# Optimization experiments

Measured on AMD Instinct MI355X. Metric: run time of the kernel, lower is better.

Reference implementation:

```python
import jax, jax.numpy as jnp
import numpy as np

B, T, E, A = 4, 4096, 1024, 1024

def setup_inputs() -> dict:
    key = jax.random.key(0)
    k1, k2, k3, k4 = jax.random.split(key, 4)
    scale = 1.0 / np.sqrt(E)  # ~ nn.Linear default init scale
    return {
        "embedded": jax.random.normal(k1, (B, T, E), dtype=jnp.float32),
        "Wq": jax.random.uniform(k2, (A, E), jnp.float32, -scale, scale),
        "Wk": jax.random.uniform(k3, (A, E), jnp.float32, -scale, scale),
        "Wv": jax.random.uniform(k4, (A, E), jnp.float32, -scale, scale),
    }

def reference(embedded, Wq, Wk, Wv):
    # QKV projections (nn.Linear without bias: x @ W.T)
    q = jnp.einsum('bte,ae->bta', embedded, Wq)
    k = jnp.einsum('bte,ae->bta', embedded, Wk)
    v = jnp.einsum('bte,ae->bta', embedded, Wv)
    A_dim = q.shape[-1]
    # scaled scores [B, T, T]
    scores = jnp.einsum('bqa,bka->bqk', q, k) / jnp.sqrt(jnp.float32(A_dim))
    # causal mask (lower triangular allowed)
    Tq = scores.shape[-1]
    causal = jnp.tril(jnp.ones((Tq, Tq), dtype=bool))
    scores = jnp.where(causal, scores, -jnp.inf)
    probs = jax.nn.softmax(scores, axis=-1)
    out = jnp.einsum('bqk,bka->bqa', probs, v)
    return jnp.round(out, 4)
```

## Files before the change

kernel.cpp:

```cpp
#include <hip/hip_runtime.h>
#include <hip/hip_bf16.h>

using bf16 = __hip_bfloat16;

typedef __attribute__((ext_vector_type(4))) float f32x4;
typedef __attribute__((ext_vector_type(8))) short short8;

typedef const void __attribute__((address_space(1)))* gas1_t;
typedef void __attribute__((address_space(3)))* las3_t;
#define GLDS(gp, lp) __builtin_amdgcn_global_load_lds((gas1_t)(gp), (las3_t)(lp), 16, 0, 0)

__device__ inline short f2bfbits(float f) {
  union { bf16 h; short s; } u;
  u.h = __float2bfloat16(f);
  return u.s;
}
__device__ inline float bf2f(short u) {
  unsigned x = ((unsigned)(unsigned short)u) << 16;
  float f; __builtin_memcpy(&f, &x, 4); return f;
}

__device__ inline void store_out(float* C, size_t idx, float v) { C[idx] = v; }
__device__ inline void store_out(bf16* C, size_t idx, float v) { C[idx] = __float2bfloat16(v); }

template<typename TOUT, int MODE>
__global__ __launch_bounds__(512, 2) void gemm256(
    const short* __restrict__ A, int lda, size_t sAz,
    const short* __restrict__ B, int ldb, size_t sBz,
    TOUT* __restrict__ C, int ldc, size_t sCz,
    int K, float scale)
{
  int bx, by;
  if constexpr (MODE == 1) {
    const int i = blockIdx.x;
    by = (int)((__builtin_sqrtf(8.f * (float)i + 1.f) - 1.f) * 0.5f);
    if (((by * (by + 1)) >> 1) > i) by--;
    else if ((((by + 1) * (by + 2)) >> 1) <= i) by++;
    bx = i - ((by * (by + 1)) >> 1);
  } else {
    bx = blockIdx.x; by = blockIdx.y;
  }
  const int z = blockIdx.z;
  const int tri_by = (by * (by + 1)) >> 1;

  A += (size_t)z * sAz;
  B += (size_t)z * sBz;
  C += (size_t)z * sCz;

  const int NT = K >> 5;

  __shared__ short As[3][256 * 32];
  __shared__ short Bs[3][256 * 32];

  const int t = threadIdx.x;
  const int lane = t & 63;
  const int wave = t >> 6;
  const int wm = wave >> 2;
  const int wn = wave & 3;
  const int fr = lane & 15, kh = lane >> 4;
  const int koff = ((kh ^ ((fr >> 1) & 3)) << 3);

  int srow[2], scol[2];
  #pragma unroll
  for (int j = 0; j < 2; j++) {
    int e = j * 512 + t;
    srow[j] = e >> 2;
    scol[j] = (((e & 3) ^ ((e >> 3) & 3)) << 3);
  }

  f32x4 acc[8][4];
  #pragma unroll
  for (int i = 0; i < 8; i++)
    #pragma unroll
    for (int j = 0; j < 4; j++) acc[i][j] = (f32x4){0.f, 0.f, 0.f, 0.f};

  auto STAGE_A = [&](int kt) {
    const int buf = kt % 3, k0 = kt * 32;
    #pragma unroll
    for (int j = 0; j < 2; j++) {
      const short* pa = A + (size_t)(by * 256 + srow[j]) * lda + k0 + scol[j];
      GLDS(pa, (char*)&As[buf][0] + j * 8192 + wave * 1024);
    }
  };
  auto STAGE_B = [&](int kt) {
    const int buf = kt % 3, k0 = kt * 32;
    #pragma unroll
    for (int j = 0; j < 2; j++) {
      const short* pb = B + (size_t)(bx * 256 + srow[j]) * ldb + k0 + scol[j];
      GLDS(pb, (char*)&Bs[buf][0] + j * 8192 + wave * 1024);
    }
  };

  STAGE_A(0); STAGE_B(0);
  STAGE_A(1); STAGE_B(1);
  asm volatile("s_waitcnt vmcnt(4)\ns_barrier" ::: "memory");

  const int arow = wm * 128 + fr;
  const int brow = wn * 64 + fr;

  for (int kt = 0; kt < NT; kt++) {
    const short* as = &As[kt % 3][0];
    const short* bs = &Bs[kt % 3][0];
    short8 af[4], bfr[4];

    #pragma unroll
    for (int n = 0; n < 4; n++) bfr[n] = *(const short8*)&bs[(brow + n * 16) * 32 + koff];
    #pragma unroll
    for (int m = 0; m < 4; m++) af[m] = *(const short8*)&as[(arow + m * 16) * 32 + koff];
    if (kt + 2 < NT) STAGE_A(kt + 2);
    __builtin_amdgcn_s_barrier();
    asm volatile("s_waitcnt lgkmcnt(0)" ::: "memory");
    __builtin_amdgcn_sched_barrier(0);
    __builtin_amdgcn_s_setprio(1);
    #pragma unroll
    for (int m = 0; m < 4; m++)
      #pragma unroll
      for (int n = 0; n < 4; n++)
        acc[m][n] = __builtin_amdgcn_mfma_f32_16x16x32_bf16(af[m], bfr[n], acc[m][n], 0, 0, 0);
    __builtin_amdgcn_s_setprio(0);
    __builtin_amdgcn_sched_barrier(0);

    #pragma unroll
    for (int m = 0; m < 4; m++) af[m] = *(const short8*)&as[(arow + (m + 4) * 16) * 32 + koff];
    if (kt + 2 < NT) STAGE_B(kt + 2);
    __builtin_amdgcn_s_barrier();
    asm volatile("s_waitcnt lgkmcnt(0)" ::: "memory");
    __builtin_amdgcn_sched_barrier(0);
    __builtin_amdgcn_s_setprio(1);
    #pragma unroll
    for (int m = 0; m < 4; m++)
      #pragma unroll
      for (int n = 0; n < 4; n++)
        acc[m + 4][n] = __builtin_amdgcn_mfma_f32_16x16x32_bf16(af[m], bfr[n], acc[m + 4][n], 0, 0, 0);
    __builtin_amdgcn_s_setprio(0);
    __builtin_amdgcn_sched_barrier(0);

    if (kt + 2 < NT)      asm volatile("s_waitcnt vmcnt(4)\ns_barrier" ::: "memory");
    else if (kt + 1 < NT) asm volatile("s_waitcnt vmcnt(0)\ns_barrier" ::: "memory");
  }

  #pragma unroll
  for (int m = 0; m < 8; m++)
    #pragma unroll
    for (int n = 0; n < 4; n++) {
      int col_l = wn * 64 + n * 16 + fr;
      #pragma unroll
      for (int r = 0; r < 4; r++) {
        int row_l = wm * 128 + m * 16 + kh * 4 + r;
        if constexpr (MODE == 1)
          store_out(C, (size_t)(tri_by + bx) * 65536 + (size_t)row_l * 256 + col_l,
                    acc[m][n][r] * scale);
        else
          store_out(C, (size_t)(by * 256 + row_l) * ldc + bx * 256 + col_l,
                    acc[m][n][r] * scale);
      }
    }
}

__global__ __launch_bounds__(512, 2) void gemm_pv_bal(
    const short* __restrict__ SP, const short* __restrict__ Vt,
    float* __restrict__ Out, float* __restrict__ Ppart)
{
  const int w = blockIdx.x;
  const int combo = w >> 4;
  const int slot = w & 15;
  const int bx = combo & 3, z = combo >> 2;
  const short* Abase = SP + (size_t)z * 136 * 65536;

  __shared__ short As[3][256 * 32];
  __shared__ short Bs[3][256 * 32];

  const int t = threadIdx.x;
  const int lane = t & 63;
  const int wave = t >> 6;
  const int wm = wave >> 2;
  const int wn = wave & 3;
  const int fr = lane & 15, kh = lane >> 4;
  const int koff = ((kh ^ ((fr >> 1) & 3)) << 3);

  int srow[2], scol[2];
  #pragma unroll
  for (int j = 0; j < 2; j++) {
    int e = j * 512 + t;
    srow[j] = e >> 2;
    scol[j] = (((e & 3) ^ ((e >> 3) & 3)) << 3);
  }
  const int arow = wm * 128 + fr;
  const int brow = wn * 64 + fr;

  const int nchunk = (slot >= 9) ? 2 : 1;
  for (int c = 0; c < nchunk; c++) {
    int by, u0, u1, pp;
    if (c == 1)            { by = slot - 9;  u0 = 0; u1 = slot - 8; pp = -1; }
    else if (slot < 8)     { by = 8 + slot;  u0 = 0; u1 = 9;        pp = -1; }
    else if (slot == 8)    { by = 7;         u0 = 0; u1 = 8;        pp = -1; }
    else                   { by = 24 - slot; u0 = 9; u1 = by + 1;   pp = slot - 9; }
    const int tri_by = (by * (by + 1)) >> 1;
    const int kt0 = u0 * 8, kt1 = u1 * 8;

    f32x4 acc[8][4];
    #pragma unroll
    for (int i = 0; i < 8; i++)
      #pragma unroll
      for (int j = 0; j < 4; j++) acc[i][j] = (f32x4){0.f, 0.f, 0.f, 0.f};

    auto STAGE_A = [&](int kt) {
      const int buf = kt % 3, k0 = kt * 32;
      #pragma unroll
      for (int j = 0; j < 2; j++) {
        const short* pa = Abase + (size_t)(tri_by + (k0 >> 8)) * 65536
                                + (size_t)srow[j] * 256 + (k0 & 255) + scol[j];
        GLDS(pa, (char*)&As[buf][0] + j * 8192 + wave * 1024);
      }
    };
    auto STAGE_B = [&](int kt) {
      const int buf = kt % 3, k0 = kt * 32;
      #pragma unroll
      for (int j = 0; j < 2; j++) {
        const short* pb = Vt + (size_t)(bx * 256 + srow[j]) * 16384 + z * 4096 + k0 + scol[j];
        GLDS(pb, (char*)&Bs[buf][0] + j * 8192 + wave * 1024);
      }
    };

    STAGE_A(kt0); STAGE_B(kt0);
    STAGE_A(kt0 + 1); STAGE_B(kt0 + 1);
    asm volatile("s_waitcnt vmcnt(4)\ns_barrier" ::: "memory");

    for (int kt = kt0; kt < kt1; kt++) {
      const short* as = &As[kt % 3][0];
      const short* bs = &Bs[kt % 3][0];
      short8 af[4], bfr[4];

      #pragma unroll
      for (int n = 0; n < 4; n++) bfr[n] = *(const short8*)&bs[(brow + n * 16) * 32 + koff];
      #pragma unroll
      for (int m = 0; m < 4; m++) af[m] = *(const short8*)&as[(arow + m * 16) * 32 + koff];
      if (kt + 2 < kt1) STAGE_A(kt + 2);
      __builtin_amdgcn_s_barrier();
      asm volatile("s_waitcnt lgkmcnt(0)" ::: "memory");
      __builtin_amdgcn_sched_barrier(0);
      __builtin_amdgcn_s_setprio(1);
      #pragma unroll
      for (int m = 0; m < 4; m++)
        #pragma unroll
        for (int n = 0; n < 4; n++)
          acc[m][n] = __builtin_amdgcn_mfma_f32_16x16x32_bf16(af[m], bfr[n], acc[m][n], 0, 0, 0);
      __builtin_amdgcn_s_setprio(0);
      __builtin_amdgcn_sched_barrier(0);

      #pragma unroll
      for (int m = 0; m < 4; m++) af[m] = *(const short8*)&as[(arow + (m + 4) * 16) * 32 + koff];
      if (kt + 2 < kt1) STAGE_B(kt + 2);
      __builtin_amdgcn_s_barrier();
      asm volatile("s_waitcnt lgkmcnt(0)" ::: "memory");
      __builtin_amdgcn_sched_barrier(0);
      __builtin_amdgcn_s_setprio(1);
      #pragma unroll
      for (int m = 0; m < 4; m++)
        #pragma unroll
        for (int n = 0; n < 4; n++)
          acc[m + 4][n] = __builtin_amdgcn_mfma_f32_16x16x32_bf16(af[m], bfr[n], acc[m + 4][n], 0, 0, 0);
      __builtin_amdgcn_s_setprio(0);
      __builtin_amdgcn_sched_barrier(0);

      if (kt + 2 < kt1)      asm volatile("s_waitcnt vmcnt(4)\ns_barrier" ::: "memory");
      else                   asm volatile("s_waitcnt vmcnt(0)\ns_barrier" ::: "memory");
    }

    #pragma unroll
    for (int m = 0; m < 8; m++)
      #pragma unroll
      for (int n = 0; n < 4; n++) {
        int col_l = wn * 64 + n * 16 + fr;
        #pragma unroll
        for (int r = 0; r < 4; r++) {
          int row_l = wm * 128 + m * 16 + kh * 4 + r;
          if (pp >= 0)
            Ppart[(size_t)(combo * 7 + pp) * 65536 + (size_t)row_l * 256 + col_l] = acc[m][n][r];
          else
            Out[(size_t)z * 4096 * 1024 + (size_t)(by * 256 + row_l) * 1024
                + bx * 256 + col_l] = acc[m][n][r];
        }
      }
    __builtin_amdgcn_s_barrier();
  }
}

__global__ __launch_bounds__(256) void pv_reduce(
    const float* __restrict__ Ppart, float* __restrict__ Out)
{
  const int u = blockIdx.x;
  const int rg = blockIdx.y;
  const int combo = u / 7, p = u % 7;
  const int by = 15 - p, bx = combo & 3, z = combo >> 2;
  const int t = threadIdx.x;
  const float* src = Ppart + (size_t)u * 65536 + (size_t)rg * 32 * 256;
  float* dst = Out + (size_t)z * 4096 * 1024
                   + (size_t)(by * 256 + rg * 32) * 1024 + bx * 256;
  for (int i = t * 4; i < 8192; i += 1024) {
    int row = i >> 8, col = i & 255;
    f32x4 a = *(const f32x4*)&src[i];
    float* d = &dst[(size_t)row * 1024 + col];
    f32x4 b = *(const f32x4*)d;
    b[0] += a[0]; b[1] += a[1]; b[2] += a[2]; b[3] += a[3];
    *(f32x4*)d = b;
  }
}

__global__ __launch_bounds__(256) void gemm128(
    const short* __restrict__ A, int lda,
    const short* __restrict__ B, int ldb,
    bf16* __restrict__ C, int ldc, int K, float scale)
{
  const int bx = blockIdx.x, by = blockIdx.y;
  __shared__ short a_lds[128 * 32];
  __shared__ short b_lds[128 * 32];

  const int t = threadIdx.x;
  const int lane = t & 63;
  const int wave = t >> 6;
  const int wm = wave >> 1, wn = wave & 1;
  const int fr = lane & 15, kh = lane >> 4;

  f32x4 acc[4][4];
  #pragma unroll
  for (int i = 0; i < 4; i++)
    #pragma unroll
    for (int j = 0; j < 4; j++) acc[i][j] = (f32x4){0.f, 0.f, 0.f, 0.f};

  for (int k0 = 0; k0 < K; k0 += 32) {
    #pragma unroll
    for (int i = 0; i < 2; i++) {
      int e = i * 256 + t;
      int r_ = e >> 2, c_ = (e & 3) * 8;
      GLDS(A + (size_t)(by * 128 + r_) * lda + k0 + c_, (char*)a_lds + i * 4096 + wave * 1024);
      GLDS(B + (size_t)(bx * 128 + r_) * ldb + k0 + c_, (char*)b_lds + i * 4096 + wave * 1024);
    }
    __syncthreads();

    short8 af[4], bfr[4];
    #pragma unroll
    for (int m = 0; m < 4; m++)
      af[m] = *(const short8*)&a_lds[(wm * 64 + m * 16 + fr) * 32 + kh * 8];
    #pragma unroll
    for (int n = 0; n < 4; n++)
      bfr[n] = *(const short8*)&b_lds[(wn * 64 + n * 16 + fr) * 32 + kh * 8];
    #pragma unroll
    for (int m = 0; m < 4; m++)
      #pragma unroll
      for (int n = 0; n < 4; n++)
        acc[m][n] = __builtin_amdgcn_mfma_f32_16x16x32_bf16(af[m], bfr[n], acc[m][n], 0, 0, 0);
    __syncthreads();
  }

  #pragma unroll
  for (int m = 0; m < 4; m++)
    #pragma unroll
    for (int n = 0; n < 4; n++) {
      int col = bx * 128 + wn * 64 + n * 16 + fr;
      #pragma unroll
      for (int r = 0; r < 4; r++) {
        int row = by * 128 + wm * 64 + m * 16 + kh * 4 + r;
        C[(size_t)row * ldc + col] = __float2bfloat16(acc[m][n][r] * scale);
      }
    }
}

__global__ __launch_bounds__(256) void cvt_bf16(
    const float* __restrict__ in, bf16* __restrict__ out, int n, float scale)
{
  for (int i = (blockIdx.x * 256 + threadIdx.x) * 8; i < n; i += gridDim.x * 2048) {
    f32x4 v0 = *(const f32x4*)&in[i];
    f32x4 v1 = *(const f32x4*)&in[i + 4];
    short8 o = { f2bfbits(v0[0] * scale), f2bfbits(v0[1] * scale),
                 f2bfbits(v0[2] * scale), f2bfbits(v0[3] * scale),
                 f2bfbits(v1[0] * scale), f2bfbits(v1[1] * scale),
                 f2bfbits(v1[2] * scale), f2bfbits(v1[3] * scale) };
    *(short8*)&out[i] = o;
  }
}

__global__ __launch_bounds__(256) void cvt_t_bf16(
    const float* __restrict__ in, bf16* __restrict__ out, int N)
{
  __shared__ float tile[64][65];
  const int bx = blockIdx.x, by = blockIdx.y;
  const int t = threadIdx.x;
  #pragma unroll
  for (int i = 0; i < 16; i++) {
    int e = i * 256 + t;
    int r = e >> 6, c = e & 63;
    tile[r][c] = in[(size_t)(by * 64 + r) * N + bx * 64 + c];
  }
  __syncthreads();
  #pragma unroll
  for (int i = 0; i < 16; i++) {
    int e = i * 256 + t;
    int r = e >> 6, c = e & 63;
    out[(size_t)(bx * 64 + r) * N + by * 64 + c] = __float2bfloat16(tile[c][r]);
  }
}

__global__ __launch_bounds__(256) void softmax_causal_packed(short* SP, int T)
{
  __shared__ float rowv[4096];
  __shared__ float red[4];
  const int r = blockIdx.x;
  const int z = blockIdx.y;
  const int rb = r >> 8, rl = r & 255;
  const size_t tri = (size_t)((rb * (rb + 1)) >> 1);
  short* base = SP + (size_t)z * 136 * 65536;
  const int L = r + 1;
  const int kend = (rb + 1) * 256;
  const int t = threadIdx.x;

  float lmax = -3.0e38f;
  for (int i = t * 8; i < kend; i += 2048) {
    short8 s = *(const short8*)(base + (tri + (i >> 8)) * 65536 + (size_t)rl * 256 + (i & 255));
    #pragma unroll
    for (int j = 0; j < 8; j++) {
      float v = bf2f(s[j]);
      rowv[i + j] = v;
      if (i + j < L) lmax = fmaxf(lmax, v);
    }
  }
  #pragma unroll
  for (int o = 32; o > 0; o >>= 1) lmax = fmaxf(lmax, __shfl_down(lmax, o));
  if ((t & 63) == 0) red[t >> 6] = lmax;
  __syncthreads();
  const float m = fmaxf(fmaxf(red[0], red[1]), fmaxf(red[2], red[3]));
  __syncthreads();

  float lsum = 0.f;
  for (int i = t * 4; i < kend; i += 1024) {
    f32x4 v = *(const f32x4*)&rowv[i];
    f32x4 e;
    #pragma unroll
    for (int j = 0; j < 4; j++)
      e[j] = (i + j < L) ? __expf(v[j] - m) : 0.f;
    *(f32x4*)&rowv[i] = e;
    lsum += e[0] + e[1] + e[2] + e[3];
  }
  #pragma unroll
  for (int o = 32; o > 0; o >>= 1) lsum += __shfl_down(lsum, o);
  if ((t & 63) == 0) red[t >> 6] = lsum;
  __syncthreads();
  const float inv = 1.f / (red[0] + red[1] + red[2] + red[3]);

  for (int i = t * 8; i < kend; i += 2048) {
    short8 o;
    #pragma unroll
    for (int j = 0; j < 8; j++) o[j] = f2bfbits(rowv[i + j] * inv);
    *(short8*)(base + (tri + (i >> 8)) * 65536 + (size_t)rl * 256 + (i & 255)) = o;
  }
}

extern "C" void kernel_launch(void* const* d_in, const int* in_sizes, int n_in,
                              void* d_out, int out_size, void* d_ws, size_t ws_size,
                              hipStream_t stream) {
  (void)in_sizes; (void)n_in; (void)out_size; (void)ws_size;
  const float* X  = (const float*)d_in[0];
  const float* Wq = (const float*)d_in[1];
  const float* Wk = (const float*)d_in[2];
  const float* Wv = (const float*)d_in[3];
  float* Out = (float*)d_out;

  const int Bn = 4, T = 4096, E = 1024, Ad = 1024;
  const int M = Bn * T;

  char* ws = (char*)d_ws;
  short* Q2  = (short*)ws;
  short* Vt  = (short*)(ws + 33554432);
  short* Xb  = (short*)(ws + 67108864);
  short* WqT = (short*)(ws + 100663296);
  short* WkT = (short*)(ws + 102760448);
  short* Wvb = (short*)(ws + 104857600);
  short* W2T = (short*)(ws + 106954752);
  short* SP  = (short*)(ws + 109051904);
  float* Ppart = (float*)ws;

  dim3 blk(256), blk5(512);
  const size_t SPz = (size_t)136 * 65536;

  cvt_bf16<<<dim3(8192), blk, 0, stream>>>(X, (bf16*)Xb, M * E, 1.0f);
  cvt_t_bf16<<<dim3(16, 16), blk, 0, stream>>>(Wq, (bf16*)WqT, E);
  cvt_t_bf16<<<dim3(16, 16), blk, 0, stream>>>(Wk, (bf16*)WkT, E);
  cvt_bf16<<<dim3(512), blk, 0, stream>>>(Wv, (bf16*)Wvb, Ad * E, 1.0f);

  gemm128<<<dim3(8, 8), blk, 0, stream>>>(
      WkT, Ad, WqT, Ad, (bf16*)W2T, E, Ad, 0.03125f);

  gemm256<bf16, 0><<<dim3(1024 / 256, M / 256), blk5, 0, stream>>>(
      Xb, E, 0, W2T, E, 0, (bf16*)Q2, 1024, 0, E, 1.0f);

  gemm256<bf16, 0><<<dim3(M / 256, Ad / 256), blk5, 0, stream>>>(
      Wvb, E, 0, Xb, E, 0, (bf16*)Vt, M, 0, E, 1.0f);

  gemm256<bf16, 1><<<dim3(136, 1, Bn), blk5, 0, stream>>>(
      Q2, 1024, (size_t)T * 1024,
      Xb, 1024, (size_t)T * 1024,
      (bf16*)SP, 256, SPz, E, 1.0f);

  softmax_causal_packed<<<dim3(T, Bn), blk, 0, stream>>>(SP, T);

  gemm_pv_bal<<<dim3(256), blk5, 0, stream>>>(SP, Vt, Out, Ppart);
  pv_reduce<<<dim3(112, 8), blk, 0, stream>>>(Ppart, Out);
}
```

Baseline: 367.1 us.

## Load-balance causal QK^T GEMM across 256 persistent blocks with split-K tail

```diff
diff --git a/kernel.cpp b/kernel.cpp
--- a/kernel.cpp
+++ b/kernel.cpp
@@ -22,6 +22,13 @@
 
 __device__ inline void store_out(float* C, size_t idx, float v) { C[idx] = v; }
 __device__ inline void store_out(bf16* C, size_t idx, float v) { C[idx] = __float2bfloat16(v); }
+
+__device__ inline void tri_decode(int i, int& by, int& bx) {
+  by = (int)((__builtin_sqrtf(8.f * (float)i + 1.f) - 1.f) * 0.5f);
+  if (((by * (by + 1)) >> 1) > i) by--;
+  else if ((((by + 1) * (by + 2)) >> 1) <= i) by++;
+  bx = i - ((by * (by + 1)) >> 1);
+}
 
 template<typename TOUT, int MODE>
 __global__ __launch_bounds__(512, 2) void gemm256(
@@ -30,18 +37,8 @@
     TOUT* __restrict__ C, int ldc, size_t sCz,
     int K, float scale)
 {
-  int bx, by;
-  if constexpr (MODE == 1) {
-    const int i = blockIdx.x;
-    by = (int)((__builtin_sqrtf(8.f * (float)i + 1.f) - 1.f) * 0.5f);
-    if (((by * (by + 1)) >> 1) > i) by--;
-    else if ((((by + 1) * (by + 2)) >> 1) <= i) by++;
-    bx = i - ((by * (by + 1)) >> 1);
-  } else {
-    bx = blockIdx.x; by = blockIdx.y;
-  }
+  const int bx = blockIdx.x, by = blockIdx.y;
   const int z = blockIdx.z;
-  const int tri_by = (by * (by + 1)) >> 1;
 
   A += (size_t)z * sAz;
   B += (size_t)z * sBz;
@@ -147,14 +144,164 @@
       #pragma unroll
       for (int r = 0; r < 4; r++) {
         int row_l = wm * 128 + m * 16 + kh * 4 + r;
-        if constexpr (MODE == 1)
-          store_out(C, (size_t)(tri_by + bx) * 65536 + (size_t)row_l * 256 + col_l,
-                    acc[m][n][r] * scale);
-        else
-          store_out(C, (size_t)(by * 256 + row_l) * ldc + bx * 256 + col_l,
-                    acc[m][n][r] * scale);
-      }
-    }
+        store_out(C, (size_t)(by * 256 + row_l) * ldc + bx * 256 + col_l,
+                  acc[m][n][r] * scale);
+      }
+    }
+}
+
+__global__ __launch_bounds__(512, 2) void gemm_s_bal(
+    const short* __restrict__ Q2, const short* __restrict__ Xb,
+    short* __restrict__ SP, float* __restrict__ Spart)
+{
+  const int b = blockIdx.x;
+  const bool haspiece = (b >= 96 && b < 160);
+  const int nchunk = haspiece ? 3 : 2;
+
+  __shared__ short As[3][256 * 32];
+  __shared__ short Bs[3][256 * 32];
+
+  const int t = threadIdx.x;
+  const int lane = t & 63;
+  const int wave = t >> 6;
+  const int wm = wave >> 2;
+  const int wn = wave & 3;
+  const int fr = lane & 15, kh = lane >> 4;
+  const int koff = ((kh ^ ((fr >> 1) & 3)) << 3);
+
+  int srow[2], scol[2];
+  #pragma unroll
+  for (int j = 0; j < 2; j++) {
+    int e = j * 512 + t;
+    srow[j] = e >> 2;
+    scol[j] = (((e & 3) ^ ((e >> 3) & 3)) << 3);
+  }
+  const int arow = wm * 128 + fr;
+  const int brow = wn * 64 + fr;
+
+  for (int c = 0; c < nchunk; c++) {
+    int tid, kt0, kt1, pp;
+    if (c < 2)       { tid = 2 * b + c;              kt0 = 0;  kt1 = 32;       pp = -1; }
+    else             { int p = b - 96; tid = 512 + (p >> 1);
+                       kt0 = (p & 1) * 16;           kt1 = kt0 + 16;           pp = p;  }
+    const int z = tid / 136, i = tid % 136;
+    int by, bx;
+    tri_decode(i, by, bx);
+    const int tri_by = (by * (by + 1)) >> 1;
+
+    const short* A = Q2 + (size_t)z * 4096 * 1024;
+    const short* B = Xb + (size_t)z * 4096 * 1024;
+
+    f32x4 acc[8][4];
+    #pragma unroll
+    for (int ii = 0; ii < 8; ii++)
+      #pragma unroll
+      for (int j = 0; j < 4; j++) acc[ii][j] = (f32x4){0.f, 0.f, 0.f, 0.f};
+
+    auto STAGE_A = [&](int kt) {
+      const int buf = kt % 3, k0 = kt * 32;
+      #pragma unroll
+      for (int j = 0; j < 2; j++) {
+        const short* pa = A + (size_t)(by * 256 + srow[j]) * 1024 + k0 + scol[j];
+        GLDS(pa, (char*)&As[buf][0] + j * 8192 + wave * 1024);
+      }
+    };
+    auto STAGE_B = [&](int kt) {
+      const int buf = kt % 3, k0 = kt * 32;
+      #pragma unroll
+      for (int j = 0; j < 2; j++) {
+        const short* pb = B + (size_t)(bx * 256 + srow[j]) * 1024 + k0 + scol[j];
+        GLDS(pb, (char*)&Bs[buf][0] + j * 8192 + wave * 1024);
+      }
+    };
+
+    STAGE_A(kt0); STAGE_B(kt0);
+    STAGE_A(kt0 + 1); STAGE_B(kt0 + 1);
+    asm volatile("s_waitcnt vmcnt(4)\ns_barrier" ::: "memory");
+
+    for (int kt = kt0; kt < kt1; kt++) {
+      const short* as = &As[kt % 3][0];
+      const short* bs = &Bs[kt % 3][0];
+      short8 af[4], bfr[4];
+
+      #pragma unroll
+      for (int n = 0; n < 4; n++) bfr[n] = *(const short8*)&bs[(brow + n * 16) * 32 + koff];
+      #pragma unroll
+      for (int m = 0; m < 4; m++) af[m] = *(const short8*)&as[(arow + m * 16) * 32 + koff];
+      if (kt + 2 < kt1) STAGE_A(kt + 2);
+      __builtin_amdgcn_s_barrier();
+      asm volatile("s_waitcnt lgkmcnt(0)" ::: "memory");
+      __builtin_amdgcn_sched_barrier(0);
+      __builtin_amdgcn_s_setprio(1);
+      #pragma unroll
+      for (int m = 0; m < 4; m++)
+        #pragma unroll
+        for (int n = 0; n < 4; n++)
+          acc[m][n] = __builtin_amdgcn_mfma_f32_16x16x32_bf16(af[m], bfr[n], acc[m][n], 0, 0, 0);
+      __builtin_amdgcn_s_setprio(0);
+      __builtin_amdgcn_sched_barrier(0);
+
+      #pragma unroll
+      for (int m = 0; m < 4; m++) af[m] = *(const short8*)&as[(arow + (m + 4) * 16) * 32 + koff];
+      if (kt + 2 < kt1) STAGE_B(kt + 2);
+      __builtin_amdgcn_s_barrier();
+      asm volatile("s_waitcnt lgkmcnt(0)" ::: "memory");
+      __builtin_amdgcn_sched_barrier(0);
+      __builtin_amdgcn_s_setprio(1);
+      #pragma unroll
+      for (int m = 0; m < 4; m++)
+        #pragma unroll
+        for (int n = 0; n < 4; n++)
+          acc[m + 4][n] = __builtin_amdgcn_mfma_f32_16x16x32_bf16(af[m], bfr[n], acc[m + 4][n], 0, 0, 0);
+      __builtin_amdgcn_s_setprio(0);
+      __builtin_amdgcn_sched_barrier(0);
+
+      if (kt + 2 < kt1)      asm volatile("s_waitcnt vmcnt(4)\ns_barrier" ::: "memory");
+      else                   asm volatile("s_waitcnt vmcnt(0)\ns_barrier" ::: "memory");
+    }
+
+    #pragma unroll
+    for (int m = 0; m < 8; m++)
+      #pragma unroll
+      for (int n = 0; n < 4; n++) {
+        int col_l = wn * 64 + n * 16 + fr;
+        #pragma unroll
+        for (int r = 0; r < 4; r++) {
+          int row_l = wm * 128 + m * 16 + kh * 4 + r;
+          if (pp >= 0)
+            Spart[(size_t)pp * 65536 + (size_t)row_l * 256 + col_l] = acc[m][n][r];
+          else
+            SP[(size_t)z * 136 * 65536 + (size_t)(tri_by + bx) * 65536
+               + (size_t)row_l * 256 + col_l] = f2bfbits(acc[m][n][r]);
+        }
+      }
+    __builtin_amdgcn_s_barrier();
+  }
+}
+
+__global__ __launch_bounds__(256) void s_reduce(
+    const float* __restrict__ Spart, short* __restrict__ SP)
+{
+  const int j = blockIdx.x, rg = blockIdx.y;
+  const int tid = 512 + j;
+  const int z = tid / 136, i = tid % 136;
+  int by, bx;
+  tri_decode(i, by, bx);
+  const int tri_by = (by * (by + 1)) >> 1;
+  const int t = threadIdx.x;
+  const float* h0 = Spart + (size_t)(2 * j) * 65536 + (size_t)rg * 32 * 256;
+  const float* h1 = h0 + 65536;
+  short* dst = SP + (size_t)z * 136 * 65536 + (size_t)(tri_by + bx) * 65536
+                  + (size_t)rg * 32 * 256;
+  for (int e = t * 4; e < 8192; e += 1024) {
+    f32x4 a = *(const f32x4*)&h0[e];
+    f32x4 b = *(const f32x4*)&h1[e];
+    short o[4];
+    #pragma unroll
+    for (int q = 0; q < 4; q++) o[q] = f2bfbits(a[q] + b[q]);
+    *(short*)&dst[e]     = o[0];
+    dst[e + 1] = o[1]; dst[e + 2] = o[2]; dst[e + 3] = o[3];
+  }
 }
 
 __global__ __launch_bounds__(512, 2) void gemm_pv_bal(
@@ -477,6 +624,7 @@
   short* Wvb = (short*)(ws + 104857600);
   short* W2T = (short*)(ws + 106954752);
   short* SP  = (short*)(ws + 109051904);
+  float* Spart = (float*)(ws + 180355072);
   float* Ppart = (float*)ws;
 
   dim3 blk(256), blk5(512);
@@ -496,10 +644,8 @@
   gemm256<bf16, 0><<<dim3(M / 256, Ad / 256), blk5, 0, stream>>>(
       Wvb, E, 0, Xb, E, 0, (bf16*)Vt, M, 0, E, 1.0f);
 
-  gemm256<bf16, 1><<<dim3(136, 1, Bn), blk5, 0, stream>>>(
-      Q2, 1024, (size_t)T * 1024,
-      Xb, 1024, (size_t)T * 1024,
-      (bf16*)SP, 256, SPz, E, 1.0f);
+  gemm_s_bal<<<dim3(256), blk5, 0, stream>>>(Q2, Xb, SP, Spart);
+  s_reduce<<<dim3(32, 8), blk, 0, stream>>>(Spart, SP);
 
   softmax_causal_packed<<<dim3(T, Bn), blk, 0, stream>>>(SP, T);
 
```

Result: slower. 377.7 us (+2.9%).
